# Performance work log

Measured on AMD Instinct MI355X. Metric: run time of the kernel, lower is better.

The kernel has to match this reference:

```python
import jax, jax.numpy as jnp
import numpy as np

N = 100_000      # nodes
E = 1_600_000    # edges (avg degree 16)
D_IN, D_H, D_OUT = 128, 128, 64


def setup_inputs() -> dict:
    key = jax.random.key(0)
    ks = jax.random.split(key, 6)
    x = jax.random.normal(ks[0], (N, D_IN), jnp.float32)
    edge_index = jax.random.randint(ks[1], (2, E), 0, N, dtype=jnp.int32)
    W1 = jax.random.normal(ks[2], (D_IN, D_H), jnp.float32) / np.sqrt(D_IN)
    b1 = jnp.zeros((D_H,), jnp.float32)
    W2 = jax.random.normal(ks[3], (D_H, D_OUT), jnp.float32) / np.sqrt(D_H)
    b2 = jnp.zeros((D_OUT,), jnp.float32)
    return {"x": x, "edge_index": edge_index, "W1": W1, "b1": b1, "W2": W2, "b2": b2}


def _gcn_layer(x, W, b, src, dst, n_nodes):
    # PyG GCNConv: h = x @ W; symmetric norm with self-loops; scatter-add; + bias
    h = x @ W                                        # [N, D_out]
    deg = jax.ops.segment_sum(jnp.ones_like(dst, jnp.float32), dst,
                              num_segments=n_nodes)  # self-loops => deg >= 1
    dinv = jax.lax.rsqrt(deg)                        # deg^{-1/2}
    norm = dinv[src] * dinv[dst]                     # [E+N]
    msg = h[src] * norm[:, None]                     # gather + scale
    out = jax.ops.segment_sum(msg, dst, num_segments=n_nodes)  # scatter-add
    return out + b


def reference(x, edge_index, W1, b1, W2, b2):
    n = x.shape[0]
    loop = jnp.arange(n, dtype=edge_index.dtype)
    src = jnp.concatenate([edge_index[0], loop])     # add self-loops
    dst = jnp.concatenate([edge_index[1], loop])
    h = _gcn_layer(x, W1, b1, src, dst, n)
    h = jax.nn.relu(h)
    # dropout(p=0.5) is identity in eval mode
    out = _gcn_layer(h, W2, b2, src, dst, n)
    return out
```

## Files before the change

kernel.cpp:

```cpp
#include <hip/hip_runtime.h>
#include <hip/hip_bf16.h>


#define NTHREADS 256
#define BSH 8
#define NBMAX 512
#define BCAP 5632
#define FC_CAP 8192

typedef unsigned int uint;
typedef unsigned short ushort;
typedef __attribute__((ext_vector_type(8))) short short8;
typedef __attribute__((ext_vector_type(4))) float floatx4;

__device__ __forceinline__ uint pack_bf16(float a, float b) {
    __hip_bfloat162 h = __float22bfloat162_rn(make_float2(a, b));
    return *reinterpret_cast<uint*>(&h);
}
__device__ __forceinline__ float bf16_lo(uint q) { return __uint_as_float(q << 16); }
__device__ __forceinline__ float bf16_hi(uint q) { return __uint_as_float(q & 0xffff0000u); }

__global__ __launch_bounds__(256) void part_gemm1(
    const int* __restrict__ src, const int* __restrict__ dst,
    int* __restrict__ bfill, uint* __restrict__ staged, int e, int nb, int eblocks,
    const float* __restrict__ X, const float* __restrict__ W1,
    uint* __restrict__ hq, int n) {
    __shared__ __align__(16) char smem[49152];
    int t = threadIdx.x;

    if ((int)blockIdx.x < eblocks) {
        uint* eP = (uint*)smem;
        ushort* eB = (ushort*)(smem + 8192);
        int* hist = (int*)(smem + 12288);
        int* base = (int*)(smem + 14336);
        int e0 = blockIdx.x * 2048;

        for (int b = t; b < nb; b += 256) hist[b] = 0;
        __syncthreads();
#pragma unroll
        for (int v = 0; v < 2; v++) {
            int li = t * 8 + v * 4;
            int gi = e0 + li;
            int4 s4, d4;
            if (gi + 3 < e) {
                s4 = *(const int4*)&src[gi];
                d4 = *(const int4*)&dst[gi];
            } else {
                const int* sp = &src[gi];
                const int* dp = &dst[gi];
                s4.x = (gi + 0 < e) ? sp[0] : 0;  d4.x = (gi + 0 < e) ? dp[0] : -1;
                s4.y = (gi + 1 < e) ? sp[1] : 0;  d4.y = (gi + 1 < e) ? dp[1] : -1;
                s4.z = (gi + 2 < e) ? sp[2] : 0;  d4.z = (gi + 2 < e) ? dp[2] : -1;
                s4.w = (gi + 3 < e) ? sp[3] : 0;  d4.w = (gi + 3 < e) ? dp[3] : -1;
            }
            uint4 p4;
            p4.x = ((uint)s4.x << 8) | ((uint)d4.x & 255u);
            p4.y = ((uint)s4.y << 8) | ((uint)d4.y & 255u);
            p4.z = ((uint)s4.z << 8) | ((uint)d4.z & 255u);
            p4.w = ((uint)s4.w << 8) | ((uint)d4.w & 255u);
            *(uint4*)&eP[li] = p4;
            eB[li + 0] = (d4.x >= 0) ? (ushort)(d4.x >> BSH) : (ushort)0xFFFF;
            eB[li + 1] = (d4.y >= 0) ? (ushort)(d4.y >> BSH) : (ushort)0xFFFF;
            eB[li + 2] = (d4.z >= 0) ? (ushort)(d4.z >> BSH) : (ushort)0xFFFF;
            eB[li + 3] = (d4.w >= 0) ? (ushort)(d4.w >> BSH) : (ushort)0xFFFF;
            if (d4.x >= 0) atomicAdd(&hist[d4.x >> BSH], 1);
            if (d4.y >= 0) atomicAdd(&hist[d4.y >> BSH], 1);
            if (d4.z >= 0) atomicAdd(&hist[d4.z >> BSH], 1);
            if (d4.w >= 0) atomicAdd(&hist[d4.w >> BSH], 1);
        }
        __syncthreads();
        for (int b = t; b < nb; b += 256) {
            int v = hist[b];
            base[b] = v ? (b * BCAP + atomicAdd(&bfill[b], v)) : 0;
            hist[b] = 0;
        }
        __syncthreads();
#pragma unroll
        for (int i = 0; i < 8; i++) {
            int li = t + i * 256;
            ushort bb = eB[li];
            if (bb != (ushort)0xFFFF) {
                int r = atomicAdd(&hist[bb], 1);
                staged[base[bb] + r] = eP[li];
            }
        }
    } else {
        ushort* sX = (ushort*)smem;
        ushort* sWT = (ushort*)(smem + 16384);
        int rbase = ((int)blockIdx.x - eblocks) * 64;

#pragma unroll
        for (int i = 0; i < 8; i++) {
            int f = t + 256 * i;
            int r = f >> 5;
            int c4 = f & 31;
            float4 v = make_float4(0.f, 0.f, 0.f, 0.f);
            int gr = rbase + r;
            if (gr < n) v = *(const float4*)(X + (size_t)gr * 128 + c4 * 4);
            uint lo = pack_bf16(v.x, v.y);
            uint hi = pack_bf16(v.z, v.w);
            int chunk = c4 >> 1;
            int sub = (c4 & 1) * 4;
            int off = r * 128 + (((chunk ^ (r & 15)) << 3) + sub);
            *(uint2*)&sX[off] = make_uint2(lo, hi);
        }
#pragma unroll
        for (int i = 0; i < 8; i++) {
            int u = t + 256 * i;
            int kp = u >> 5;
            int n4 = u & 31;
            int k = kp * 2;
            float4 w0 = *(const float4*)(W1 + (size_t)k * 128 + n4 * 4);
            float4 w1 = *(const float4*)(W1 + (size_t)(k + 1) * 128 + n4 * 4);
            int chunk = k >> 3;
            int sub = k & 7;
            const float* a0 = (const float*)&w0;
            const float* a1 = (const float*)&w1;
#pragma unroll
            for (int j = 0; j < 4; j++) {
                int nn = n4 * 4 + j;
                uint pk = pack_bf16(a0[j], a1[j]);
                int off = nn * 128 + (((chunk ^ (nn & 15)) << 3) + sub);
                *(uint*)&sWT[off] = pk;
            }
        }
        __syncthreads();

        int lane = t & 63;
        int wave = t >> 6;
        int m = lane & 15;
        int q = lane >> 4;
        int r0 = wave * 16;

        floatx4 acc[8];
#pragma unroll
        for (int c = 0; c < 8; c++) acc[c] = (floatx4){0.f, 0.f, 0.f, 0.f};

#pragma unroll
        for (int ks = 0; ks < 4; ks++) {
            int rr = r0 + m;
            int ca = (ks * 4 + q) ^ (rr & 15);
            short8 afrag = *(const short8*)&sX[rr * 128 + (ca << 3)];
#pragma unroll
            for (int c = 0; c < 8; c++) {
                int nn = c * 16 + m;
                int cb = (ks * 4 + q) ^ (nn & 15);
                short8 bfrag = *(const short8*)&sWT[nn * 128 + (cb << 3)];
                acc[c] = __builtin_amdgcn_mfma_f32_16x16x32_bf16(bfrag, afrag, acc[c], 0, 0, 0);
            }
        }

        int gr = rbase + r0 + m;
        if (gr < n) {
#pragma unroll
            for (int c = 0; c < 8; c++) {
                uint2 pk;
                pk.x = pack_bf16(acc[c][0], acc[c][1]);
                pk.y = pack_bf16(acc[c][2], acc[c][3]);
                *(uint2*)&hq[(size_t)gr * 64 + c * 8 + q * 2] = pk;
            }
        }
    }
}

__global__ __launch_bounds__(256) void fine_csr_kernel(
    const uint* __restrict__ staged, const int* __restrict__ bfill,
    int4* __restrict__ meta, float* __restrict__ dinv,
    int* __restrict__ rec, int n) {
    __shared__ uint eL[FC_CAP];
    __shared__ int lcnt[256];
    __shared__ int tsum[256];
    __shared__ int red[256];
    int b = blockIdx.x;
    int t = threadIdx.x;

    int part = 0;
    for (int j = t; j < b; j += 256) part += bfill[j];
    red[t] = part;
    lcnt[t] = 0;
    __syncthreads();
    for (int off = 128; off > 0; off >>= 1) {
        if (t < off) red[t] += red[t + off];
        __syncthreads();
    }
    int s0 = red[0];
    int m = bfill[b];

    int sb = b * BCAP;
    for (int i = t; i < m; i += 256) {
        uint pk = staged[sb + i];
        eL[i] = pk;
        atomicAdd(&lcnt[pk & 255u], 1);
    }
    __syncthreads();
    int v = lcnt[t];
    tsum[t] = v;
    __syncthreads();
    int x = v;
    for (int off = 1; off < 256; off <<= 1) {
        int y = (t >= off) ? tsum[t - off] : 0;
        __syncthreads();
        x += y;
        tsum[t] = x;
        __syncthreads();
    }
    int excl = x - v;
    int node = (b << BSH) + t;
    if (node < n) {
        float di = rsqrtf((float)v + 1.0f);
        dinv[node] = di;
        meta[node] = make_int4(s0 + excl, v, __float_as_int(di), __float_as_int(di * di));
    }
    lcnt[t] = s0 + excl;
    __syncthreads();
    for (int i = t; i < m; i += 256) {
        uint pk = eL[i];
        int pos = atomicAdd(&lcnt[pk & 255u], 1);
        rec[pos] = (int)(pk >> 8);
    }
}

__global__ __launch_bounds__(512) void agg128_mm64(
    const uint* __restrict__ hq, const int* __restrict__ rec,
    const int4* __restrict__ meta, const float* __restrict__ dinv,
    const float* __restrict__ bias, const float* __restrict__ W2,
    uint* __restrict__ h2q, int n) {
    __shared__ ushort sWT[64 * 128];
    __shared__ ushort sg[32 * 128];
    int t = threadIdx.x;

#pragma unroll
    for (int i = 0; i < 2; i++) {
        int u = t + 512 * i;
        int kp = u >> 4;
        int n4 = u & 15;
        int k = kp * 2;
        float4 w0 = *(const float4*)(W2 + (size_t)k * 64 + n4 * 4);
        float4 w1 = *(const float4*)(W2 + (size_t)(k + 1) * 64 + n4 * 4);
        int chunk = k >> 3;
        int sub = k & 7;
        const float* a0f = (const float*)&w0;
        const float* a1f = (const float*)&w1;
#pragma unroll
        for (int j = 0; j < 4; j++) {
            int nn = n4 * 4 + j;
            uint pk = pack_bf16(a0f[j], a1f[j]);
            *(uint*)&sWT[nn * 128 + (((chunk ^ (nn & 15)) << 3) + sub)] = pk;
        }
    }

    int qw = t >> 4;
    int fl = t & 15;
    int nb0 = blockIdx.x * 32;
    int w = nb0 + qw;
    bool valid = w < n;
    int wsafe = valid ? w : 0;
    const uint4* h4 = (const uint4*)hq;

    int4 mt = meta[wsafe];
    int j0 = mt.x;
    int deg = valid ? mt.y : 0;
    float di = __int_as_float(mt.z);
    float swq = valid ? __int_as_float(mt.w) : 0.f;

    uint4 qs = h4[(size_t)wsafe * 16 + fl];
    float a0 = bf16_lo(qs.x) * swq, a1 = bf16_hi(qs.x) * swq;
    float a2 = bf16_lo(qs.y) * swq, a3 = bf16_hi(qs.y) * swq;
    float a4 = bf16_lo(qs.z) * swq, a5 = bf16_hi(qs.z) * swq;
    float a6 = bf16_lo(qs.w) * swq, a7 = bf16_hi(qs.w) * swq;

    const int* rp = rec + j0;
    int tt = 0;
    for (; tt + 8 <= deg; tt += 8) {
        int s[8]; float wf[8]; uint4 q[8];
#pragma unroll
        for (int u = 0; u < 8; u++) s[u] = rp[tt + u];
#pragma unroll
        for (int u = 0; u < 8; u++) wf[u] = dinv[s[u]] * di;
#pragma unroll
        for (int u = 0; u < 8; u++) q[u] = h4[(size_t)s[u] * 16 + fl];
#pragma unroll
        for (int u = 0; u < 8; u++) {
            a0 += bf16_lo(q[u].x) * wf[u]; a1 += bf16_hi(q[u].x) * wf[u];
            a2 += bf16_lo(q[u].y) * wf[u]; a3 += bf16_hi(q[u].y) * wf[u];
            a4 += bf16_lo(q[u].z) * wf[u]; a5 += bf16_hi(q[u].z) * wf[u];
            a6 += bf16_lo(q[u].w) * wf[u]; a7 += bf16_hi(q[u].w) * wf[u];
        }
    }
    for (; tt + 2 <= deg; tt += 2) {
        int s0i = rp[tt], s1i = rp[tt + 1];
        float w0v = dinv[s0i] * di, w1v = dinv[s1i] * di;
        uint4 q0 = h4[(size_t)s0i * 16 + fl];
        uint4 q1 = h4[(size_t)s1i * 16 + fl];
        a0 += bf16_lo(q0.x) * w0v + bf16_lo(q1.x) * w1v;
        a1 += bf16_hi(q0.x) * w0v + bf16_hi(q1.x) * w1v;
        a2 += bf16_lo(q0.y) * w0v + bf16_lo(q1.y) * w1v;
        a3 += bf16_hi(q0.y) * w0v + bf16_hi(q1.y) * w1v;
        a4 += bf16_lo(q0.z) * w0v + bf16_lo(q1.z) * w1v;
        a5 += bf16_hi(q0.z) * w0v + bf16_hi(q1.z) * w1v;
        a6 += bf16_lo(q0.w) * w0v + bf16_lo(q1.w) * w1v;
        a7 += bf16_hi(q0.w) * w0v + bf16_hi(q1.w) * w1v;
    }
    if (tt < deg) {
        int s = rp[tt];
        float wv = dinv[s] * di;
        uint4 q0 = h4[(size_t)s * 16 + fl];
        a0 += bf16_lo(q0.x) * wv; a1 += bf16_hi(q0.x) * wv;
        a2 += bf16_lo(q0.y) * wv; a3 += bf16_hi(q0.y) * wv;
        a4 += bf16_lo(q0.z) * wv; a5 += bf16_hi(q0.z) * wv;
        a6 += bf16_lo(q0.w) * wv; a7 += bf16_hi(q0.w) * wv;
    }

    float4 bb0 = *(const float4*)&bias[8 * fl];
    float4 bb1 = *(const float4*)&bias[8 * fl + 4];
    uint4 pkv;
    pkv.x = pack_bf16(fmaxf(a0 + bb0.x, 0.f), fmaxf(a1 + bb0.y, 0.f));
    pkv.y = pack_bf16(fmaxf(a2 + bb0.z, 0.f), fmaxf(a3 + bb0.w, 0.f));
    pkv.z = pack_bf16(fmaxf(a4 + bb1.x, 0.f), fmaxf(a5 + bb1.y, 0.f));
    pkv.w = pack_bf16(fmaxf(a6 + bb1.z, 0.f), fmaxf(a7 + bb1.w, 0.f));
    *(uint4*)&sg[qw * 128 + ((fl ^ (qw & 15)) << 3)] = pkv;
    __syncthreads();

    int wave = t >> 6;
    int lane = t & 63;
    int m = lane & 15;
    int qq = lane >> 4;
    int rt = wave >> 2;
    int ct = wave & 3;
    floatx4 acc = (floatx4){0.f, 0.f, 0.f, 0.f};
#pragma unroll
    for (int ks = 0; ks < 4; ks++) {
        int rr = rt * 16 + m;
        int ca = (ks * 4 + qq) ^ (rr & 15);
        short8 afrag = *(const short8*)&sg[rr * 128 + (ca << 3)];
        int nn = ct * 16 + m;
        int cb = (ks * 4 + qq) ^ (nn & 15);
        short8 bfrag = *(const short8*)&sWT[nn * 128 + (cb << 3)];
        acc = __builtin_amdgcn_mfma_f32_16x16x32_bf16(bfrag, afrag, acc, 0, 0, 0);
    }
    int gr = nb0 + rt * 16 + m;
    if (gr < n) {
        float sc = dinv[gr];
        uint2 pk;
        pk.x = pack_bf16(acc[0] * sc, acc[1] * sc);
        pk.y = pack_bf16(acc[2] * sc, acc[3] * sc);
        *(uint2*)&h2q[(size_t)gr * 32 + ct * 8 + qq * 2] = pk;
    }
}

__global__ __launch_bounds__(256) void aggregate64q(
    const uint* __restrict__ hq, const int* __restrict__ rec,
    const int4* __restrict__ meta, const float* __restrict__ bias,
    float* __restrict__ out, int n) {
    int gt = blockIdx.x * 256 + threadIdx.x;
    int w = gt >> 3;
    if (w >= n) return;
    int fl = gt & 7;

    int4 mt = meta[w];
    int j0 = mt.x;
    int deg = mt.y;
    float di = __int_as_float(mt.z);
    const uint4* h4 = (const uint4*)hq;

    uint4 qs = h4[(size_t)w * 8 + fl];
    float a0 = bf16_lo(qs.x), a1 = bf16_hi(qs.x);
    float a2 = bf16_lo(qs.y), a3 = bf16_hi(qs.y);
    float a4 = bf16_lo(qs.z), a5 = bf16_hi(qs.z);
    float a6 = bf16_lo(qs.w), a7 = bf16_hi(qs.w);

    const int* rp = rec + j0;
    int tt = 0;
    for (; tt + 8 <= deg; tt += 8) {
        int s[8]; uint4 q[8];
#pragma unroll
        for (int u = 0; u < 8; u++) s[u] = rp[tt + u];
#pragma unroll
        for (int u = 0; u < 8; u++) q[u] = h4[(size_t)s[u] * 8 + fl];
#pragma unroll
        for (int u = 0; u < 8; u++) {
            a0 += bf16_lo(q[u].x); a1 += bf16_hi(q[u].x);
            a2 += bf16_lo(q[u].y); a3 += bf16_hi(q[u].y);
            a4 += bf16_lo(q[u].z); a5 += bf16_hi(q[u].z);
            a6 += bf16_lo(q[u].w); a7 += bf16_hi(q[u].w);
        }
    }
    for (; tt + 2 <= deg; tt += 2) {
        int s0i = rp[tt], s1i = rp[tt + 1];
        uint4 q0 = h4[(size_t)s0i * 8 + fl];
        uint4 q1 = h4[(size_t)s1i * 8 + fl];
        a0 += bf16_lo(q0.x) + bf16_lo(q1.x);
        a1 += bf16_hi(q0.x) + bf16_hi(q1.x);
        a2 += bf16_lo(q0.y) + bf16_lo(q1.y);
        a3 += bf16_hi(q0.y) + bf16_hi(q1.y);
        a4 += bf16_lo(q0.z) + bf16_lo(q1.z);
        a5 += bf16_hi(q0.z) + bf16_hi(q1.z);
        a6 += bf16_lo(q0.w) + bf16_lo(q1.w);
        a7 += bf16_hi(q0.w) + bf16_hi(q1.w);
    }
    if (tt < deg) {
        int s = rp[tt];
        uint4 q0 = h4[(size_t)s * 8 + fl];
        a0 += bf16_lo(q0.x); a1 += bf16_hi(q0.x);
        a2 += bf16_lo(q0.y); a3 += bf16_hi(q0.y);
        a4 += bf16_lo(q0.z); a5 += bf16_hi(q0.z);
        a6 += bf16_lo(q0.w); a7 += bf16_hi(q0.w);
    }

    float4 bb0 = *(const float4*)&bias[8 * fl];
    float4 bb1 = *(const float4*)&bias[8 * fl + 4];
    float4 o0, o1;
    o0.x = di * a0 + bb0.x; o0.y = di * a1 + bb0.y;
    o0.z = di * a2 + bb0.z; o0.w = di * a3 + bb0.w;
    o1.x = di * a4 + bb1.x; o1.y = di * a5 + bb1.y;
    o1.z = di * a6 + bb1.z; o1.w = di * a7 + bb1.w;
    *(float4*)&out[(size_t)w * 64 + 8 * fl] = o0;
    *(float4*)&out[(size_t)w * 64 + 8 * fl + 4] = o1;
}

extern "C" void kernel_launch(void* const* d_in, const int* in_sizes, int n_in,
                              void* d_out, int out_size, void* d_ws, size_t ws_size,
                              hipStream_t stream) {
    const float* x = (const float*)d_in[0];
    const int* edge = (const int*)d_in[1];
    const float* W1 = (const float*)d_in[2];
    const float* b1 = (const float*)d_in[3];
    const float* W2 = (const float*)d_in[4];
    const float* b2 = (const float*)d_in[5];

    const int N = in_sizes[0] / 128;
    const int E = in_sizes[1] / 2;
    const int* src = edge;
    const int* dst = edge + E;
    const int NB = (N + (1 << BSH) - 1) >> BSH;

    char* p = (char*)d_ws;
    int* bfill = (int*)p;     p += NBMAX * 4;
    float* dinv = (float*)p;  p += (size_t)N * 4;
    int4* meta = (int4*)p;    p += (size_t)N * 16;
    int* rec = (int*)p;       p += (size_t)E * 4;
    uint* staged = (uint*)p;  p += (size_t)NBMAX * BCAP * 4;
    uint* hq = (uint*)p;      p += (size_t)N * 64 * 4;
    uint* h2q = (uint*)p;     p += (size_t)N * 32 * 4;

    float* out = (float*)d_out;
    const int eblocks = (E + 2047) / 2048;
    const int gblocks = (N + 63) / 64;

    (void)hipMemsetAsync(bfill, 0, NBMAX * 4, stream);
    part_gemm1<<<eblocks + gblocks, 256, 0, stream>>>(
        src, dst, bfill, staged, E, NB, eblocks, x, W1, hq, N);
    fine_csr_kernel<<<NB, 256, 0, stream>>>(staged, bfill, meta, dinv, rec, N);
    agg128_mm64<<<(N + 31) / 32, 512, 0, stream>>>(hq, rec, meta, dinv, b1, W2, h2q, N);
    aggregate64q<<<(N * 8 + 255) / 256, 256, 0, stream>>>(h2q, rec, meta, b2, out, N);
}
```

Before: 267.9 us.

## Fuse GCN pipeline into one persistent kernel with software grid barriers

Replaces the four separate launches (partition+GEMM1, CSR build, layer-1 aggregate+GEMM2, layer-2 aggregate) with a single persistent kernel sized from occupancy. Phases are separated by an atomic-counter grid barrier, and work items are strided across the resident blocks. The aim is to remove launch gaps and inter-kernel drain/fill bubbles. In exchange it relies on all blocks being co-resident, and it changes the block size to 512 along with the per-phase work split. Spin-barrier overhead and lower per-phase occupancy may offset the gains.

```diff
diff --git a/kernel.cpp b/kernel.cpp
--- a/kernel.cpp
+++ b/kernel.cpp
@@ -2,11 +2,10 @@
 #include <hip/hip_bf16.h>
 
 
-#define NTHREADS 256
 #define BSH 8
 #define NBMAX 512
 #define BCAP 5632
-#define FC_CAP 8192
+#define MT 512
 
 typedef unsigned int uint;
 typedef unsigned short ushort;
@@ -20,402 +19,432 @@
 __device__ __forceinline__ float bf16_lo(uint q) { return __uint_as_float(q << 16); }
 __device__ __forceinline__ float bf16_hi(uint q) { return __uint_as_float(q & 0xffff0000u); }
 
-__global__ __launch_bounds__(256) void part_gemm1(
+__device__ __forceinline__ void grid_sync(int* cnt, int* gen, int nb) {
+    __syncthreads();
+    if (threadIdx.x == 0) {
+        __threadfence();
+        int g = __hip_atomic_load(gen, __ATOMIC_RELAXED, __HIP_MEMORY_SCOPE_AGENT);
+        int tk = __hip_atomic_fetch_add(cnt, 1, __ATOMIC_ACQ_REL, __HIP_MEMORY_SCOPE_AGENT);
+        if (tk == nb - 1) {
+            __hip_atomic_store(cnt, 0, __ATOMIC_RELAXED, __HIP_MEMORY_SCOPE_AGENT);
+            __hip_atomic_store(gen, g + 1, __ATOMIC_RELEASE, __HIP_MEMORY_SCOPE_AGENT);
+        } else {
+            while (__hip_atomic_load(gen, __ATOMIC_ACQUIRE, __HIP_MEMORY_SCOPE_AGENT) == g)
+                __builtin_amdgcn_s_sleep(8);
+        }
+        __threadfence();
+    }
+    __syncthreads();
+}
+
+__global__ __launch_bounds__(MT) void gcn_mega(
     const int* __restrict__ src, const int* __restrict__ dst,
-    int* __restrict__ bfill, uint* __restrict__ staged, int e, int nb, int eblocks,
     const float* __restrict__ X, const float* __restrict__ W1,
-    uint* __restrict__ hq, int n) {
-    __shared__ __align__(16) char smem[49152];
+    const float* __restrict__ b1, const float* __restrict__ W2,
+    const float* __restrict__ b2,
+    int* __restrict__ bfill, int* __restrict__ bar,
+    uint* __restrict__ staged, int4* __restrict__ meta,
+    float* __restrict__ dinv, int* __restrict__ rec,
+    uint* __restrict__ hq, uint* __restrict__ h2q,
+    float* __restrict__ out,
+    int e, int n, int nb, int pitems, int gitems, int citems, int ditems) {
+    __shared__ __attribute__((aligned(16))) char smem[35840];
     int t = threadIdx.x;
-
-    if ((int)blockIdx.x < eblocks) {
+    const int G = gridDim.x;
+    int* bcnt = bar;
+    int* bgen = bar + 1;
+
+    {
         uint* eP = (uint*)smem;
-        ushort* eB = (ushort*)(smem + 8192);
-        int* hist = (int*)(smem + 12288);
-        int* base = (int*)(smem + 14336);
-        int e0 = blockIdx.x * 2048;
-
-        for (int b = t; b < nb; b += 256) hist[b] = 0;
+        ushort* eB = (ushort*)(smem + 16384);
+        int* hist = (int*)(smem + 24576);
+        int* base = (int*)(smem + 26624);
+        for (int it = blockIdx.x; it < pitems; it += G) {
+            __syncthreads();
+            int e0 = it * 4096;
+            for (int b = t; b < nb; b += MT) hist[b] = 0;
+            __syncthreads();
+#pragma unroll
+            for (int v = 0; v < 2; v++) {
+                int li = t * 8 + v * 4;
+                int gi = e0 + li;
+                int4 s4, d4;
+                if (gi + 3 < e) {
+                    s4 = *(const int4*)&src[gi];
+                    d4 = *(const int4*)&dst[gi];
+                } else {
+                    const int* sp = &src[gi];
+                    const int* dp = &dst[gi];
+                    s4.x = (gi + 0 < e) ? sp[0] : 0;  d4.x = (gi + 0 < e) ? dp[0] : -1;
+                    s4.y = (gi + 1 < e) ? sp[1] : 0;  d4.y = (gi + 1 < e) ? dp[1] : -1;
+                    s4.z = (gi + 2 < e) ? sp[2] : 0;  d4.z = (gi + 2 < e) ? dp[2] : -1;
+                    s4.w = (gi + 3 < e) ? sp[3] : 0;  d4.w = (gi + 3 < e) ? dp[3] : -1;
+                }
+                uint4 p4;
+                p4.x = ((uint)s4.x << 8) | ((uint)d4.x & 255u);
+                p4.y = ((uint)s4.y << 8) | ((uint)d4.y & 255u);
+                p4.z = ((uint)s4.z << 8) | ((uint)d4.z & 255u);
+                p4.w = ((uint)s4.w << 8) | ((uint)d4.w & 255u);
+                *(uint4*)&eP[li] = p4;
+                eB[li + 0] = (d4.x >= 0) ? (ushort)(d4.x >> BSH) : (ushort)0xFFFF;
+                eB[li + 1] = (d4.y >= 0) ? (ushort)(d4.y >> BSH) : (ushort)0xFFFF;
+                eB[li + 2] = (d4.z >= 0) ? (ushort)(d4.z >> BSH) : (ushort)0xFFFF;
+                eB[li + 3] = (d4.w >= 0) ? (ushort)(d4.w >> BSH) : (ushort)0xFFFF;
+                if (d4.x >= 0) atomicAdd(&hist[d4.x >> BSH], 1);
+                if (d4.y >= 0) atomicAdd(&hist[d4.y >> BSH], 1);
+                if (d4.z >= 0) atomicAdd(&hist[d4.z >> BSH], 1);
+                if (d4.w >= 0) atomicAdd(&hist[d4.w >> BSH], 1);
+            }
+            __syncthreads();
+            for (int b = t; b < nb; b += MT) {
+                int v = hist[b];
+                base[b] = v ? (b * BCAP + atomicAdd(&bfill[b], v)) : 0;
+                hist[b] = 0;
+            }
+            __syncthreads();
+#pragma unroll
+            for (int i = 0; i < 8; i++) {
+                int li = t + i * MT;
+                ushort bb = eB[li];
+                if (bb != (ushort)0xFFFF) {
+                    int r = atomicAdd(&hist[bb], 1);
+                    staged[base[bb] + r] = eP[li];
+                }
+            }
+        }
+    }
+    grid_sync(bcnt, bgen, G);
+
+    {
+        int btot = nb + gitems;
+        for (int it = blockIdx.x; it < btot; it += G) {
+            if (it < nb) {
+                uint* eL = (uint*)smem;
+                int* lcnt = (int*)(smem + 32768);
+                int* ts = (int*)(smem + 33792);
+                int b = it;
+                __syncthreads();
+                int part = 0;
+                for (int j = t; j < b; j += MT) part += bfill[j];
+                ts[t] = part;
+                if (t < 256) lcnt[t] = 0;
+                __syncthreads();
+                for (int off = 256; off > 0; off >>= 1) {
+                    if (t < off) ts[t] += ts[t + off];
+                    __syncthreads();
+                }
+                int s0 = ts[0];
+                int m = bfill[b];
+                int sb = b * BCAP;
+                __syncthreads();
+                for (int i = t; i < m; i += MT) {
+                    uint pk = staged[sb + i];
+                    eL[i] = pk;
+                    atomicAdd(&lcnt[pk & 255u], 1);
+                }
+                __syncthreads();
+                int v = 0, x = 0;
+                if (t < 256) { v = lcnt[t]; ts[t] = v; x = v; }
+                __syncthreads();
+                for (int off = 1; off < 256; off <<= 1) {
+                    int y = 0;
+                    if (t < 256 && t >= off) y = ts[t - off];
+                    __syncthreads();
+                    if (t < 256) { x += y; ts[t] = x; }
+                    __syncthreads();
+                }
+                if (t < 256) {
+                    int excl = x - v;
+                    int node = (b << BSH) + t;
+                    if (node < n) {
+                        float di = rsqrtf((float)v + 1.0f);
+                        dinv[node] = di;
+                        meta[node] = make_int4(s0 + excl, v, __float_as_int(di),
+                                               __float_as_int(di * di));
+                    }
+                    lcnt[t] = s0 + excl;
+                }
+                __syncthreads();
+                for (int i = t; i < m; i += MT) {
+                    uint pk = eL[i];
+                    int pos = atomicAdd(&lcnt[pk & 255u], 1);
+                    rec[pos] = (int)(pk >> 8);
+                }
+            } else {
+                ushort* sX = (ushort*)smem;
+                ushort* sWT = (ushort*)(smem + 16384);
+                int rbase = (it - nb) * 64;
+                __syncthreads();
+#pragma unroll
+                for (int i = 0; i < 4; i++) {
+                    int f = t + MT * i;
+                    int r = f >> 5;
+                    int c4 = f & 31;
+                    float4 v = make_float4(0.f, 0.f, 0.f, 0.f);
+                    int gr = rbase + r;
+                    if (gr < n) v = *(const float4*)(X + (size_t)gr * 128 + c4 * 4);
+                    uint lo = pack_bf16(v.x, v.y);
+                    uint hi = pack_bf16(v.z, v.w);
+                    int chunk = c4 >> 1;
+                    int sub = (c4 & 1) * 4;
+                    int off = r * 128 + (((chunk ^ (r & 15)) << 3) + sub);
+                    *(uint2*)&sX[off] = make_uint2(lo, hi);
+                }
+                for (int ch = 0; ch < 2; ch++) {
+                    __syncthreads();
+#pragma unroll
+                    for (int i = 0; i < 2; i++) {
+                        int u = t + MT * i;
+                        int kp = u >> 4;
+                        int n4 = u & 15;
+                        int k = kp * 2;
+                        const float* w0p = W1 + (size_t)k * 128 + ch * 64 + n4 * 4;
+                        const float* w1p = W1 + (size_t)(k + 1) * 128 + ch * 64 + n4 * 4;
+                        float4 w0 = *(const float4*)w0p;
+                        float4 w1 = *(const float4*)w1p;
+                        int chunk = k >> 3;
+                        int sub = k & 7;
+                        const float* a0 = (const float*)&w0;
+                        const float* a1 = (const float*)&w1;
+#pragma unroll
+                        for (int j = 0; j < 4; j++) {
+                            int nn = n4 * 4 + j;
+                            uint pk = pack_bf16(a0[j], a1[j]);
+                            *(uint*)&sWT[nn * 128 + (((chunk ^ (nn & 15)) << 3) + sub)] = pk;
+                        }
+                    }
+                    __syncthreads();
+                    int lane = t & 63;
+                    int wave = t >> 6;
+                    int m = lane & 15;
+                    int q = lane >> 4;
+                    int rt = wave >> 1;
+                    int ctl = wave & 1;
+                    floatx4 acc[2];
+                    acc[0] = (floatx4){0.f, 0.f, 0.f, 0.f};
+                    acc[1] = (floatx4){0.f, 0.f, 0.f, 0.f};
+#pragma unroll
+                    for (int ks = 0; ks < 4; ks++) {
+                        int rr = rt * 16 + m;
+                        int ca = (ks * 4 + q) ^ (rr & 15);
+                        short8 afrag = *(const short8*)&sX[rr * 128 + (ca << 3)];
+#pragma unroll
+                        for (int c = 0; c < 2; c++) {
+                            int nn = ctl * 32 + c * 16 + m;
+                            int cb = (ks * 4 + q) ^ (nn & 15);
+                            short8 bfrag = *(const short8*)&sWT[nn * 128 + (cb << 3)];
+                            acc[c] = __builtin_amdgcn_mfma_f32_16x16x32_bf16(bfrag, afrag, acc[c], 0, 0, 0);
+                        }
+                    }
+                    int gr = rbase + rt * 16 + m;
+                    if (gr < n) {
+#pragma unroll
+                        for (int c = 0; c < 2; c++) {
+                            int T = ch * 4 + ctl * 2 + c;
+                            uint2 pk;
+                            pk.x = pack_bf16(acc[c][0], acc[c][1]);
+                            pk.y = pack_bf16(acc[c][2], acc[c][3]);
+                            *(uint2*)&hq[(size_t)gr * 64 + T * 8 + q * 2] = pk;
+                        }
+                    }
+                }
+            }
+        }
+    }
+    grid_sync(bcnt, bgen, G);
+
+    {
+        ushort* sWT = (ushort*)smem;
+        ushort* sg = (ushort*)(smem + 16384);
+        const uint4* h4 = (const uint4*)hq;
         __syncthreads();
 #pragma unroll
-        for (int v = 0; v < 2; v++) {
-            int li = t * 8 + v * 4;
-            int gi = e0 + li;
-            int4 s4, d4;
-            if (gi + 3 < e) {
-                s4 = *(const int4*)&src[gi];
-                d4 = *(const int4*)&dst[gi];
-            } else {
-                const int* sp = &src[gi];
-                const int* dp = &dst[gi];
-                s4.x = (gi + 0 < e) ? sp[0] : 0;  d4.x = (gi + 0 < e) ? dp[0] : -1;
-                s4.y = (gi + 1 < e) ? sp[1] : 0;  d4.y = (gi + 1 < e) ? dp[1] : -1;
-                s4.z = (gi + 2 < e) ? sp[2] : 0;  d4.z = (gi + 2 < e) ? dp[2] : -1;
-                s4.w = (gi + 3 < e) ? sp[3] : 0;  d4.w = (gi + 3 < e) ? dp[3] : -1;
-            }
-            uint4 p4;
-            p4.x = ((uint)s4.x << 8) | ((uint)d4.x & 255u);
-            p4.y = ((uint)s4.y << 8) | ((uint)d4.y & 255u);
-            p4.z = ((uint)s4.z << 8) | ((uint)d4.z & 255u);
-            p4.w = ((uint)s4.w << 8) | ((uint)d4.w & 255u);
-            *(uint4*)&eP[li] = p4;
-            eB[li + 0] = (d4.x >= 0) ? (ushort)(d4.x >> BSH) : (ushort)0xFFFF;
-            eB[li + 1] = (d4.y >= 0) ? (ushort)(d4.y >> BSH) : (ushort)0xFFFF;
-            eB[li + 2] = (d4.z >= 0) ? (ushort)(d4.z >> BSH) : (ushort)0xFFFF;
-            eB[li + 3] = (d4.w >= 0) ? (ushort)(d4.w >> BSH) : (ushort)0xFFFF;
-            if (d4.x >= 0) atomicAdd(&hist[d4.x >> BSH], 1);
-            if (d4.y >= 0) atomicAdd(&hist[d4.y >> BSH], 1);
-            if (d4.z >= 0) atomicAdd(&hist[d4.z >> BSH], 1);
-            if (d4.w >= 0) atomicAdd(&hist[d4.w >> BSH], 1);
-        }
-        __syncthreads();
-        for (int b = t; b < nb; b += 256) {
-            int v = hist[b];
-            base[b] = v ? (b * BCAP + atomicAdd(&bfill[b], v)) : 0;
-            hist[b] = 0;
-        }
-        __syncthreads();
-#pragma unroll
-        for (int i = 0; i < 8; i++) {
-            int li = t + i * 256;
-            ushort bb = eB[li];
-            if (bb != (ushort)0xFFFF) {
-                int r = atomicAdd(&hist[bb], 1);
-                staged[base[bb] + r] = eP[li];
-            }
-        }
-    } else {
-        ushort* sX = (ushort*)smem;
-        ushort* sWT = (ushort*)(smem + 16384);
-        int rbase = ((int)blockIdx.x - eblocks) * 64;
-
-#pragma unroll
-        for (int i = 0; i < 8; i++) {
-            int f = t + 256 * i;
-            int r = f >> 5;
-            int c4 = f & 31;
-            float4 v = make_float4(0.f, 0.f, 0.f, 0.f);
-            int gr = rbase + r;
-            if (gr < n) v = *(const float4*)(X + (size_t)gr * 128 + c4 * 4);
-            uint lo = pack_bf16(v.x, v.y);
-            uint hi = pack_bf16(v.z, v.w);
-            int chunk = c4 >> 1;
-            int sub = (c4 & 1) * 4;
-            int off = r * 128 + (((chunk ^ (r & 15)) << 3) + sub);
-            *(uint2*)&sX[off] = make_uint2(lo, hi);
-        }
-#pragma unroll
-        for (int i = 0; i < 8; i++) {
-            int u = t + 256 * i;
-            int kp = u >> 5;
-            int n4 = u & 31;
+        for (int i = 0; i < 2; i++) {
+            int u = t + MT * i;
+            int kp = u >> 4;
+            int n4 = u & 15;
             int k = kp * 2;
-            float4 w0 = *(const float4*)(W1 + (size_t)k * 128 + n4 * 4);
-            float4 w1 = *(const float4*)(W1 + (size_t)(k + 1) * 128 + n4 * 4);
+            float4 w0 = *(const float4*)(W2 + (size_t)k * 64 + n4 * 4);
+            float4 w1 = *(const float4*)(W2 + (size_t)(k + 1) * 64 + n4 * 4);
             int chunk = k >> 3;
             int sub = k & 7;
-            const float* a0 = (const float*)&w0;
-            const float* a1 = (const float*)&w1;
+            const float* a0f = (const float*)&w0;
+            const float* a1f = (const float*)&w1;
 #pragma unroll
             for (int j = 0; j < 4; j++) {
                 int nn = n4 * 4 + j;
-                uint pk = pack_bf16(a0[j], a1[j]);
-                int off = nn * 128 + (((chunk ^ (nn & 15)) << 3) + sub);
-                *(uint*)&sWT[off] = pk;
+                uint pk = pack_bf16(a0f[j], a1f[j]);
+                *(uint*)&sWT[nn * 128 + (((chunk ^ (nn & 15)) << 3) + sub)] = pk;
             }
         }
-        __syncthreads();
-
-        int lane = t & 63;
-        int wave = t >> 6;
-        int m = lane & 15;
-        int q = lane >> 4;
-        int r0 = wave * 16;
-
-        floatx4 acc[8];
-#pragma unroll
-        for (int c = 0; c < 8; c++) acc[c] = (floatx4){0.f, 0.f, 0.f, 0.f};
-
-#pragma unroll
-        for (int ks = 0; ks < 4; ks++) {
-            int rr = r0 + m;
-            int ca = (ks * 4 + q) ^ (rr & 15);
-            short8 afrag = *(const short8*)&sX[rr * 128 + (ca << 3)];
-#pragma unroll
-            for (int c = 0; c < 8; c++) {
-                int nn = c * 16 + m;
-                int cb = (ks * 4 + q) ^ (nn & 15);
+
+        int qw = t >> 4;
+        int fl = t & 15;
+        for (int it = blockIdx.x; it < citems; it += G) {
+            int nb0 = it * 32;
+            int w = nb0 + qw;
+            bool valid = w < n;
+            int wsafe = valid ? w : 0;
+            int4 mt = meta[wsafe];
+            int j0 = mt.x;
+            int deg = valid ? mt.y : 0;
+            float di = __int_as_float(mt.z);
+            float swq = valid ? __int_as_float(mt.w) : 0.f;
+
+            uint4 qs = h4[(size_t)wsafe * 16 + fl];
+            float a0 = bf16_lo(qs.x) * swq, a1 = bf16_hi(qs.x) * swq;
+            float a2 = bf16_lo(qs.y) * swq, a3 = bf16_hi(qs.y) * swq;
+            float a4 = bf16_lo(qs.z) * swq, a5 = bf16_hi(qs.z) * swq;
+            float a6 = bf16_lo(qs.w) * swq, a7 = bf16_hi(qs.w) * swq;
+
+            const int* rp = rec + j0;
+            int tt = 0;
+            for (; tt + 8 <= deg; tt += 8) {
+                int s[8]; float wf[8]; uint4 q[8];
+#pragma unroll
+                for (int u = 0; u < 8; u++) s[u] = rp[tt + u];
+#pragma unroll
+                for (int u = 0; u < 8; u++) wf[u] = dinv[s[u]] * di;
+#pragma unroll
+                for (int u = 0; u < 8; u++) q[u] = h4[(size_t)s[u] * 16 + fl];
+#pragma unroll
+                for (int u = 0; u < 8; u++) {
+                    a0 += bf16_lo(q[u].x) * wf[u]; a1 += bf16_hi(q[u].x) * wf[u];
+                    a2 += bf16_lo(q[u].y) * wf[u]; a3 += bf16_hi(q[u].y) * wf[u];
+                    a4 += bf16_lo(q[u].z) * wf[u]; a5 += bf16_hi(q[u].z) * wf[u];
+                    a6 += bf16_lo(q[u].w) * wf[u]; a7 += bf16_hi(q[u].w) * wf[u];
+                }
+            }
+            for (; tt + 2 <= deg; tt += 2) {
+                int s0i = rp[tt], s1i = rp[tt + 1];
+                float w0v = dinv[s0i] * di, w1v = dinv[s1i] * di;
+                uint4 q0 = h4[(size_t)s0i * 16 + fl];
+                uint4 q1 = h4[(size_t)s1i * 16 + fl];
+                a0 += bf16_lo(q0.x) * w0v + bf16_lo(q1.x) * w1v;
+                a1 += bf16_hi(q0.x) * w0v + bf16_hi(q1.x) * w1v;
+                a2 += bf16_lo(q0.y) * w0v + bf16_lo(q1.y) * w1v;
+                a3 += bf16_hi(q0.y) * w0v + bf16_hi(q1.y) * w1v;
+                a4 += bf16_lo(q0.z) * w0v + bf16_lo(q1.z) * w1v;
+                a5 += bf16_hi(q0.z) * w0v + bf16_hi(q1.z) * w1v;
+                a6 += bf16_lo(q0.w) * w0v + bf16_lo(q1.w) * w1v;
+                a7 += bf16_hi(q0.w) * w0v + bf16_hi(q1.w) * w1v;
+            }
+            if (tt < deg) {
+                int s = rp[tt];
+                float wv = dinv[s] * di;
+                uint4 q0 = h4[(size_t)s * 16 + fl];
+                a0 += bf16_lo(q0.x) * wv; a1 += bf16_hi(q0.x) * wv;
+                a2 += bf16_lo(q0.y) * wv; a3 += bf16_hi(q0.y) * wv;
+                a4 += bf16_lo(q0.z) * wv; a5 += bf16_hi(q0.z) * wv;
+                a6 += bf16_lo(q0.w) * wv; a7 += bf16_hi(q0.w) * wv;
+            }
+
+            float4 bb0 = *(const float4*)&b1[8 * fl];
+            float4 bb1 = *(const float4*)&b1[8 * fl + 4];
+            uint4 pkv;
+            pkv.x = pack_bf16(fmaxf(a0 + bb0.x, 0.f), fmaxf(a1 + bb0.y, 0.f));
+            pkv.y = pack_bf16(fmaxf(a2 + bb0.z, 0.f), fmaxf(a3 + bb0.w, 0.f));
+            pkv.z = pack_bf16(fmaxf(a4 + bb1.x, 0.f), fmaxf(a5 + bb1.y, 0.f));
+            pkv.w = pack_bf16(fmaxf(a6 + bb1.z, 0.f), fmaxf(a7 + bb1.w, 0.f));
+            __syncthreads();
+            *(uint4*)&sg[qw * 128 + ((fl ^ (qw & 15)) << 3)] = pkv;
+            __syncthreads();
+
+            int wave = t >> 6;
+            int lane = t & 63;
+            int m = lane & 15;
+            int qq = lane >> 4;
+            int rt = wave >> 2;
+            int ct = wave & 3;
+            floatx4 acc = (floatx4){0.f, 0.f, 0.f, 0.f};
+#pragma unroll
+            for (int ks = 0; ks < 4; ks++) {
+                int rr = rt * 16 + m;
+                int ca = (ks * 4 + qq) ^ (rr & 15);
+                short8 afrag = *(const short8*)&sg[rr * 128 + (ca << 3)];
+                int nn = ct * 16 + m;
+                int cb = (ks * 4 + qq) ^ (nn & 15);
                 short8 bfrag = *(const short8*)&sWT[nn * 128 + (cb << 3)];
-                acc[c] = __builtin_amdgcn_mfma_f32_16x16x32_bf16(bfrag, afrag, acc[c], 0, 0, 0);
-            }
-        }
-
-        int gr = rbase + r0 + m;
-        if (gr < n) {
-#pragma unroll
-            for (int c = 0; c < 8; c++) {
+                acc = __builtin_amdgcn_mfma_f32_16x16x32_bf16(bfrag, afrag, acc, 0, 0, 0);
+            }
+            int gr = nb0 + rt * 16 + m;
+            if (gr < n) {
+                float sc = dinv[gr];
                 uint2 pk;
-                pk.x = pack_bf16(acc[c][0], acc[c][1]);
-                pk.y = pack_bf16(acc[c][2], acc[c][3]);
-                *(uint2*)&hq[(size_t)gr * 64 + c * 8 + q * 2] = pk;
+                pk.x = pack_bf16(acc[0] * sc, acc[1] * sc);
+                pk.y = pack_bf16(acc[2] * sc, acc[3] * sc);
+                *(uint2*)&h2q[(size_t)gr * 32 + ct * 8 + qq * 2] = pk;
             }
         }
     }
-}
-
-__global__ __launch_bounds__(256) void fine_csr_kernel(
-    const uint* __restrict__ staged, const int* __restrict__ bfill,
-    int4* __restrict__ meta, float* __restrict__ dinv,
-    int* __restrict__ rec, int n) {
-    __shared__ uint eL[FC_CAP];
-    __shared__ int lcnt[256];
-    __shared__ int tsum[256];
-    __shared__ int red[256];
-    int b = blockIdx.x;
-    int t = threadIdx.x;
-
-    int part = 0;
-    for (int j = t; j < b; j += 256) part += bfill[j];
-    red[t] = part;
-    lcnt[t] = 0;
-    __syncthreads();
-    for (int off = 128; off > 0; off >>= 1) {
-        if (t < off) red[t] += red[t + off];
-        __syncthreads();
-    }
-    int s0 = red[0];
-    int m = bfill[b];
-
-    int sb = b * BCAP;
-    for (int i = t; i < m; i += 256) {
-        uint pk = staged[sb + i];
-        eL[i] = pk;
-        atomicAdd(&lcnt[pk & 255u], 1);
-    }
-    __syncthreads();
-    int v = lcnt[t];
-    tsum[t] = v;
-    __syncthreads();
-    int x = v;
-    for (int off = 1; off < 256; off <<= 1) {
-        int y = (t >= off) ? tsum[t - off] : 0;
-        __syncthreads();
-        x += y;
-        tsum[t] = x;
-        __syncthreads();
-    }
-    int excl = x - v;
-    int node = (b << BSH) + t;
-    if (node < n) {
-        float di = rsqrtf((float)v + 1.0f);
-        dinv[node] = di;
-        meta[node] = make_int4(s0 + excl, v, __float_as_int(di), __float_as_int(di * di));
-    }
-    lcnt[t] = s0 + excl;
-    __syncthreads();
-    for (int i = t; i < m; i += 256) {
-        uint pk = eL[i];
-        int pos = atomicAdd(&lcnt[pk & 255u], 1);
-        rec[pos] = (int)(pk >> 8);
-    }
-}
-
-__global__ __launch_bounds__(512) void agg128_mm64(
-    const uint* __restrict__ hq, const int* __restrict__ rec,
-    const int4* __restrict__ meta, const float* __restrict__ dinv,
-    const float* __restrict__ bias, const float* __restrict__ W2,
-    uint* __restrict__ h2q, int n) {
-    __shared__ ushort sWT[64 * 128];
-    __shared__ ushort sg[32 * 128];
-    int t = threadIdx.x;
-
-#pragma unroll
-    for (int i = 0; i < 2; i++) {
-        int u = t + 512 * i;
-        int kp = u >> 4;
-        int n4 = u & 15;
-        int k = kp * 2;
-        float4 w0 = *(const float4*)(W2 + (size_t)k * 64 + n4 * 4);
-        float4 w1 = *(const float4*)(W2 + (size_t)(k + 1) * 64 + n4 * 4);
-        int chunk = k >> 3;
-        int sub = k & 7;
-        const float* a0f = (const float*)&w0;
-        const float* a1f = (const float*)&w1;
-#pragma unroll
-        for (int j = 0; j < 4; j++) {
-            int nn = n4 * 4 + j;
-            uint pk = pack_bf16(a0f[j], a1f[j]);
-            *(uint*)&sWT[nn * 128 + (((chunk ^ (nn & 15)) << 3) + sub)] = pk;
+    grid_sync(bcnt, bgen, G);
+
+    {
+        const uint4* h4 = (const uint4*)h2q;
+        int fl = t & 7;
+        for (int it = blockIdx.x; it < ditems; it += G) {
+            int w = it * 64 + (t >> 3);
+            if (w >= n) continue;
+            int4 mt = meta[w];
+            int j0 = mt.x;
+            int deg = mt.y;
+            float di = __int_as_float(mt.z);
+
+            uint4 qs = h4[(size_t)w * 8 + fl];
+            float a0 = bf16_lo(qs.x), a1 = bf16_hi(qs.x);
+            float a2 = bf16_lo(qs.y), a3 = bf16_hi(qs.y);
+            float a4 = bf16_lo(qs.z), a5 = bf16_hi(qs.z);
+            float a6 = bf16_lo(qs.w), a7 = bf16_hi(qs.w);
+
+            const int* rp = rec + j0;
+            int tt = 0;
+            for (; tt + 8 <= deg; tt += 8) {
+                int s[8]; uint4 q[8];
+#pragma unroll
+                for (int u = 0; u < 8; u++) s[u] = rp[tt + u];
+#pragma unroll
+                for (int u = 0; u < 8; u++) q[u] = h4[(size_t)s[u] * 8 + fl];
+#pragma unroll
+                for (int u = 0; u < 8; u++) {
+                    a0 += bf16_lo(q[u].x); a1 += bf16_hi(q[u].x);
+                    a2 += bf16_lo(q[u].y); a3 += bf16_hi(q[u].y);
+                    a4 += bf16_lo(q[u].z); a5 += bf16_hi(q[u].z);
+                    a6 += bf16_lo(q[u].w); a7 += bf16_hi(q[u].w);
+                }
+            }
+            for (; tt + 2 <= deg; tt += 2) {
+                int s0i = rp[tt], s1i = rp[tt + 1];
+                uint4 q0 = h4[(size_t)s0i * 8 + fl];
+                uint4 q1 = h4[(size_t)s1i * 8 + fl];
+                a0 += bf16_lo(q0.x) + bf16_lo(q1.x);
+                a1 += bf16_hi(q0.x) + bf16_hi(q1.x);
+                a2 += bf16_lo(q0.y) + bf16_lo(q1.y);
+                a3 += bf16_hi(q0.y) + bf16_hi(q1.y);
+                a4 += bf16_lo(q0.z) + bf16_lo(q1.z);
+                a5 += bf16_hi(q0.z) + bf16_hi(q1.z);
+                a6 += bf16_lo(q0.w) + bf16_lo(q1.w);
+                a7 += bf16_hi(q0.w) + bf16_hi(q1.w);
+            }
+            if (tt < deg) {
+                int s = rp[tt];
+                uint4 q0 = h4[(size_t)s * 8 + fl];
+                a0 += bf16_lo(q0.x); a1 += bf16_hi(q0.x);
+                a2 += bf16_lo(q0.y); a3 += bf16_hi(q0.y);
+                a4 += bf16_lo(q0.z); a5 += bf16_hi(q0.z);
+                a6 += bf16_lo(q0.w); a7 += bf16_hi(q0.w);
+            }
+
+            float4 bb0 = *(const float4*)&b2[8 * fl];
+            float4 bb1 = *(const float4*)&b2[8 * fl + 4];
+            float4 o0, o1;
+            o0.x = di * a0 + bb0.x; o0.y = di * a1 + bb0.y;
+            o0.z = di * a2 + bb0.z; o0.w = di * a3 + bb0.w;
+            o1.x = di * a4 + bb1.x; o1.y = di * a5 + bb1.y;
+            o1.z = di * a6 + bb1.z; o1.w = di * a7 + bb1.w;
+            *(float4*)&out[(size_t)w * 64 + 8 * fl] = o0;
+            *(float4*)&out[(size_t)w * 64 + 8 * fl + 4] = o1;
         }
     }
-
-    int qw = t >> 4;
-    int fl = t & 15;
-    int nb0 = blockIdx.x * 32;
-    int w = nb0 + qw;
-    bool valid = w < n;
-    int wsafe = valid ? w : 0;
-    const uint4* h4 = (const uint4*)hq;
-
-    int4 mt = meta[wsafe];
-    int j0 = mt.x;
-    int deg = valid ? mt.y : 0;
-    float di = __int_as_float(mt.z);
-    float swq = valid ? __int_as_float(mt.w) : 0.f;
-
-    uint4 qs = h4[(size_t)wsafe * 16 + fl];
-    float a0 = bf16_lo(qs.x) * swq, a1 = bf16_hi(qs.x) * swq;
-    float a2 = bf16_lo(qs.y) * swq, a3 = bf16_hi(qs.y) * swq;
-    float a4 = bf16_lo(qs.z) * swq, a5 = bf16_hi(qs.z) * swq;
-    float a6 = bf16_lo(qs.w) * swq, a7 = bf16_hi(qs.w) * swq;
-
-    const int* rp = rec + j0;
-    int tt = 0;
-    for (; tt + 8 <= deg; tt += 8) {
-        int s[8]; float wf[8]; uint4 q[8];
-#pragma unroll
-        for (int u = 0; u < 8; u++) s[u] = rp[tt + u];
-#pragma unroll
-        for (int u = 0; u < 8; u++) wf[u] = dinv[s[u]] * di;
-#pragma unroll
-        for (int u = 0; u < 8; u++) q[u] = h4[(size_t)s[u] * 16 + fl];
-#pragma unroll
-        for (int u = 0; u < 8; u++) {
-            a0 += bf16_lo(q[u].x) * wf[u]; a1 += bf16_hi(q[u].x) * wf[u];
-            a2 += bf16_lo(q[u].y) * wf[u]; a3 += bf16_hi(q[u].y) * wf[u];
-            a4 += bf16_lo(q[u].z) * wf[u]; a5 += bf16_hi(q[u].z) * wf[u];
-            a6 += bf16_lo(q[u].w) * wf[u]; a7 += bf16_hi(q[u].w) * wf[u];
-        }
-    }
-    for (; tt + 2 <= deg; tt += 2) {
-        int s0i = rp[tt], s1i = rp[tt + 1];
-        float w0v = dinv[s0i] * di, w1v = dinv[s1i] * di;
-        uint4 q0 = h4[(size_t)s0i * 16 + fl];
-        uint4 q1 = h4[(size_t)s1i * 16 + fl];
-        a0 += bf16_lo(q0.x) * w0v + bf16_lo(q1.x) * w1v;
-        a1 += bf16_hi(q0.x) * w0v + bf16_hi(q1.x) * w1v;
-        a2 += bf16_lo(q0.y) * w0v + bf16_lo(q1.y) * w1v;
-        a3 += bf16_hi(q0.y) * w0v + bf16_hi(q1.y) * w1v;
-        a4 += bf16_lo(q0.z) * w0v + bf16_lo(q1.z) * w1v;
-        a5 += bf16_hi(q0.z) * w0v + bf16_hi(q1.z) * w1v;
-        a6 += bf16_lo(q0.w) * w0v + bf16_lo(q1.w) * w1v;
-        a7 += bf16_hi(q0.w) * w0v + bf16_hi(q1.w) * w1v;
-    }
-    if (tt < deg) {
-        int s = rp[tt];
-        float wv = dinv[s] * di;
-        uint4 q0 = h4[(size_t)s * 16 + fl];
-        a0 += bf16_lo(q0.x) * wv; a1 += bf16_hi(q0.x) * wv;
-        a2 += bf16_lo(q0.y) * wv; a3 += bf16_hi(q0.y) * wv;
-        a4 += bf16_lo(q0.z) * wv; a5 += bf16_hi(q0.z) * wv;
-        a6 += bf16_lo(q0.w) * wv; a7 += bf16_hi(q0.w) * wv;
-    }
-
-    float4 bb0 = *(const float4*)&bias[8 * fl];
-    float4 bb1 = *(const float4*)&bias[8 * fl + 4];
-    uint4 pkv;
-    pkv.x = pack_bf16(fmaxf(a0 + bb0.x, 0.f), fmaxf(a1 + bb0.y, 0.f));
-    pkv.y = pack_bf16(fmaxf(a2 + bb0.z, 0.f), fmaxf(a3 + bb0.w, 0.f));
-    pkv.z = pack_bf16(fmaxf(a4 + bb1.x, 0.f), fmaxf(a5 + bb1.y, 0.f));
-    pkv.w = pack_bf16(fmaxf(a6 + bb1.z, 0.f), fmaxf(a7 + bb1.w, 0.f));
-    *(uint4*)&sg[qw * 128 + ((fl ^ (qw & 15)) << 3)] = pkv;
-    __syncthreads();
-
-    int wave = t >> 6;
-    int lane = t & 63;
-    int m = lane & 15;
-    int qq = lane >> 4;
-    int rt = wave >> 2;
-    int ct = wave & 3;
-    floatx4 acc = (floatx4){0.f, 0.f, 0.f, 0.f};
-#pragma unroll
-    for (int ks = 0; ks < 4; ks++) {
-        int rr = rt * 16 + m;
-        int ca = (ks * 4 + qq) ^ (rr & 15);
-        short8 afrag = *(const short8*)&sg[rr * 128 + (ca << 3)];
-        int nn = ct * 16 + m;
-        int cb = (ks * 4 + qq) ^ (nn & 15);
-        short8 bfrag = *(const short8*)&sWT[nn * 128 + (cb << 3)];
-        acc = __builtin_amdgcn_mfma_f32_16x16x32_bf16(bfrag, afrag, acc, 0, 0, 0);
-    }
-    int gr = nb0 + rt * 16 + m;
-    if (gr < n) {
-        float sc = dinv[gr];
-        uint2 pk;
-        pk.x = pack_bf16(acc[0] * sc, acc[1] * sc);
-        pk.y = pack_bf16(acc[2] * sc, acc[3] * sc);
-        *(uint2*)&h2q[(size_t)gr * 32 + ct * 8 + qq * 2] = pk;
-    }
-}
-
-__global__ __launch_bounds__(256) void aggregate64q(
-    const uint* __restrict__ hq, const int* __restrict__ rec,
-    const int4* __restrict__ meta, const float* __restrict__ bias,
-    float* __restrict__ out, int n) {
-    int gt = blockIdx.x * 256 + threadIdx.x;
-    int w = gt >> 3;
-    if (w >= n) return;
-    int fl = gt & 7;
-
-    int4 mt = meta[w];
-    int j0 = mt.x;
-    int deg = mt.y;
-    float di = __int_as_float(mt.z);
-    const uint4* h4 = (const uint4*)hq;
-
-    uint4 qs = h4[(size_t)w * 8 + fl];
-    float a0 = bf16_lo(qs.x), a1 = bf16_hi(qs.x);
-    float a2 = bf16_lo(qs.y), a3 = bf16_hi(qs.y);
-    float a4 = bf16_lo(qs.z), a5 = bf16_hi(qs.z);
-    float a6 = bf16_lo(qs.w), a7 = bf16_hi(qs.w);
-
-    const int* rp = rec + j0;
-    int tt = 0;
-    for (; tt + 8 <= deg; tt += 8) {
-        int s[8]; uint4 q[8];
-#pragma unroll
-        for (int u = 0; u < 8; u++) s[u] = rp[tt + u];
-#pragma unroll
-        for (int u = 0; u < 8; u++) q[u] = h4[(size_t)s[u] * 8 + fl];
-#pragma unroll
-        for (int u = 0; u < 8; u++) {
-            a0 += bf16_lo(q[u].x); a1 += bf16_hi(q[u].x);
-            a2 += bf16_lo(q[u].y); a3 += bf16_hi(q[u].y);
-            a4 += bf16_lo(q[u].z); a5 += bf16_hi(q[u].z);
-            a6 += bf16_lo(q[u].w); a7 += bf16_hi(q[u].w);
-        }
-    }
-    for (; tt + 2 <= deg; tt += 2) {
-        int s0i = rp[tt], s1i = rp[tt + 1];
-        uint4 q0 = h4[(size_t)s0i * 8 + fl];
-        uint4 q1 = h4[(size_t)s1i * 8 + fl];
-        a0 += bf16_lo(q0.x) + bf16_lo(q1.x);
-        a1 += bf16_hi(q0.x) + bf16_hi(q1.x);
-        a2 += bf16_lo(q0.y) + bf16_lo(q1.y);
-        a3 += bf16_hi(q0.y) + bf16_hi(q1.y);
-        a4 += bf16_lo(q0.z) + bf16_lo(q1.z);
-        a5 += bf16_hi(q0.z) + bf16_hi(q1.z);
-        a6 += bf16_lo(q0.w) + bf16_lo(q1.w);
-        a7 += bf16_hi(q0.w) + bf16_hi(q1.w);
-    }
-    if (tt < deg) {
-        int s = rp[tt];
-        uint4 q0 = h4[(size_t)s * 8 + fl];
-        a0 += bf16_lo(q0.x); a1 += bf16_hi(q0.x);
-        a2 += bf16_lo(q0.y); a3 += bf16_hi(q0.y);
-        a4 += bf16_lo(q0.z); a5 += bf16_hi(q0.z);
-        a6 += bf16_lo(q0.w); a7 += bf16_hi(q0.w);
-    }
-
-    float4 bb0 = *(const float4*)&bias[8 * fl];
-    float4 bb1 = *(const float4*)&bias[8 * fl + 4];
-    float4 o0, o1;
-    o0.x = di * a0 + bb0.x; o0.y = di * a1 + bb0.y;
-    o0.z = di * a2 + bb0.z; o0.w = di * a3 + bb0.w;
-    o1.x = di * a4 + bb1.x; o1.y = di * a5 + bb1.y;
-    o1.z = di * a6 + bb1.z; o1.w = di * a7 + bb1.w;
-    *(float4*)&out[(size_t)w * 64 + 8 * fl] = o0;
-    *(float4*)&out[(size_t)w * 64 + 8 * fl + 4] = o1;
 }
 
 extern "C" void kernel_launch(void* const* d_in, const int* in_sizes, int n_in,
@@ -436,6 +465,7 @@
 
     char* p = (char*)d_ws;
     int* bfill = (int*)p;     p += NBMAX * 4;
+    int* bar = (int*)p;       p += 64;
     float* dinv = (float*)p;  p += (size_t)N * 4;
     int4* meta = (int4*)p;    p += (size_t)N * 16;
     int* rec = (int*)p;       p += (size_t)E * 4;
@@ -444,13 +474,30 @@
     uint* h2q = (uint*)p;     p += (size_t)N * 32 * 4;
 
     float* out = (float*)d_out;
-    const int eblocks = (E + 2047) / 2048;
-    const int gblocks = (N + 63) / 64;
-
-    (void)hipMemsetAsync(bfill, 0, NBMAX * 4, stream);
-    part_gemm1<<<eblocks + gblocks, 256, 0, stream>>>(
-        src, dst, bfill, staged, E, NB, eblocks, x, W1, hq, N);
-    fine_csr_kernel<<<NB, 256, 0, stream>>>(staged, bfill, meta, dinv, rec, N);
-    agg128_mm64<<<(N + 31) / 32, 512, 0, stream>>>(hq, rec, meta, dinv, b1, W2, h2q, N);
-    aggregate64q<<<(N * 8 + 255) / 256, 256, 0, stream>>>(h2q, rec, meta, b2, out, N);
+    const int pitems = (E + 4095) / 4096;
+    const int gitems = (N + 63) / 64;
+    const int citems = (N + 31) / 32;
+    const int ditems = (N + 63) / 64;
+
+    static int g_blocks = 0;
+    if (g_blocks == 0) {
+        int occ = 0;
+        if (hipOccupancyMaxActiveBlocksPerMultiprocessor(
+                &occ, (const void*)gcn_mega, MT, 0) != hipSuccess || occ < 1)
+            occ = 1;
+        int dev = 0;
+        (void)hipGetDevice(&dev);
+        int cus = 0;
+        if (hipDeviceGetAttribute(&cus, hipDeviceAttributeMultiprocessorCount,
+                                  dev) != hipSuccess || cus < 1)
+            cus = 256;
+        g_blocks = occ * cus;
+        if (g_blocks > 2048) g_blocks = 2048;
+    }
+
+    (void)hipMemsetAsync(bfill, 0, NBMAX * 4 + 64, stream);
+    gcn_mega<<<g_blocks, MT, 0, stream>>>(
+        src, dst, x, W1, b1, W2, b2,
+        bfill, bar, staged, meta, dinv, rec, hq, h2q, out,
+        E, N, NB, pitems, gitems, citems, ditems);
 }
```

Measured after the change: 516.9 us. +92.9%, slower.
